# Kernel optimization log

Measured on AMD Instinct MI355X. Metric: run time of the kernel, lower is better.

The kernel has to match this reference:

```python
import jax, jax.numpy as jnp
import numpy as np
from itertools import permutations

NUM_CLASSES = 6
T_ITERS = 2
IMG = (256, 256)
EPS = 1e-12


def _pad1(x):
    # ConstantPad2d(1, 1): pad spatial dims with value 1
    return jnp.pad(x, ((0, 0), (0, 0), (1, 1), (1, 1)), constant_values=1.0)


def _maxpool3(x):
    # MaxPool2d(3, stride=1, valid) then pad(1, value=1) -> same spatial size
    y = jax.lax.reduce_window(x, -jnp.inf, jax.lax.max,
                              (1, 1, 3, 3), (1, 1, 1, 1), 'VALID')
    return _pad1(y)


def _avgpool3(x):
    y = jax.lax.reduce_window(x, 0.0, jax.lax.add,
                              (1, 1, 3, 3), (1, 1, 1, 1), 'VALID') / 9.0
    return _pad1(y)


def _normalize_ch(x):
    # F.normalize(x) default: L2 over dim=1
    n = jnp.sqrt(jnp.sum(x * x, axis=1, keepdims=True))
    return x / jnp.maximum(n, EPS)


def _opening(xp):
    # xp: [B, C2, S+2, S+2]; x = matmul(maxpool(x), xp), T times
    x = xp
    for _ in range(T_ITERS):
        x = jnp.matmul(_maxpool3(x), xp)
    return x


def _rectification(original, dilated):
    off = dilated - original
    off = off - jnp.mean(off, axis=2, keepdims=True)
    return original + jax.nn.relu(off)


def _selective_dilation(xp):
    x = xp
    for _ in range(T_ITERS):
        x2 = jnp.matmul(_avgpool3(x), xp)
        x = _rectification(x, x2)
    return x


def _final_operation(fc, mode):
    if mode == 'opening':
        operand = _pad1(-fc)            # negate-then-pad (see notes re: shape fix)
        operated = _opening(_pad1(fc))
    else:
        operand = _pad1(fc)
        operated = _selective_dilation(operand)
    x = jnp.matmul(_normalize_ch(operated), operand)
    sub = operand - x
    return jnp.sum(jnp.abs(sub))        # torch.norm(p=1)


def setup_inputs() -> dict:
    key = jax.random.key(0)
    k1, k2 = jax.random.split(key)
    logits = jax.random.normal(k1, (1, NUM_CLASSES, 64, 64), dtype=jnp.float32)
    base_loss = jax.random.uniform(k2, (1,), dtype=jnp.float32)
    return {"logits": logits, "base_loss": base_loss}


def reference(logits, base_loss):
    B, C, h, w = logits.shape
    up = jax.image.resize(logits, (B, C, IMG[0], IMG[1]), method='bilinear')
    soft = jax.nn.softmax(up, axis=1)

    # permutation pairs (i, j), i != j: cat -> mean over pair -> sub -> relu
    pairs = np.array(list(permutations(range(C), 2)))  # [P, 2]
    a = soft[:, pairs[:, 0]]            # [B, P, H, W]
    b = soft[:, pairs[:, 1]]
    d = (a - b) * 0.5                   # a - mean = (a-b)/2 ; b - mean = (b-a)/2
    fc = jnp.stack([jax.nn.relu(d), jax.nn.relu(-d)], axis=2)
    fc = fc.reshape(B, 2 * pairs.shape[0], IMG[0], IMG[1])  # [B, 2P, H, W]

    n_open = _final_operation(fc, 'opening')
    n_dil = _final_operation(fc, 'dilation')
    final_norm = jnp.abs(n_open - n_dil)
    return final_norm + base_loss       # [1]
```

## Files before the change

### kernel.cpp

```cpp
#include <hip/hip_runtime.h>
#include <math.h>

#define HP 258
#define RPAD 320
#define BSTR 328
#define NPIX (HP*HP)
#define NPB  (RPAD*BSTR)
#define PTOT (RPAD*BSTR)
#define C30 30
#define TOT (C30*NPIX)
#define LOGW 64
#define PBLK 410
#define CH 3

typedef __bf16 bf16x8 __attribute__((ext_vector_type(8)));
typedef float  f32x4  __attribute__((ext_vector_type(4)));
typedef unsigned short ushort;
typedef unsigned short ushort8 __attribute__((ext_vector_type(8)));

static __device__ inline ushort f2bf(float f){
  __bf16 h = (__bf16)f;
  return __builtin_bit_cast(ushort, h);
}
static __device__ inline float bf2f(ushort u){
  return (float)__builtin_bit_cast(__bf16, u);
}

static __device__ inline int xcd_swz(int orig, int nwg){
  int xcd = orig & 7, s = orig >> 3;
  int q = nwg >> 3, r = nwg & 7;
  return (xcd < r ? xcd*(q+1) : r*(q+1) + (xcd - r)*q) + s;
}

#define MM_MFMA_72(KK)                                                         \
  {                                                                            \
    bf16x8 a0 = __builtin_bit_cast(bf16x8, *(const ushort8*)(&As[(wr      + l15)*72 + (KK) + lq*8])); \
    bf16x8 a1 = __builtin_bit_cast(bf16x8, *(const ushort8*)(&As[(wr + 16 + l15)*72 + (KK) + lq*8])); \
    bf16x8 b0 = __builtin_bit_cast(bf16x8, *(const ushort8*)(&Bs[(wc      + l15)*72 + (KK) + lq*8])); \
    bf16x8 b1 = __builtin_bit_cast(bf16x8, *(const ushort8*)(&Bs[(wc + 16 + l15)*72 + (KK) + lq*8])); \
    acc00 = __builtin_amdgcn_mfma_f32_16x16x32_bf16(a0, b0, acc00, 0, 0, 0);   \
    acc01 = __builtin_amdgcn_mfma_f32_16x16x32_bf16(a0, b1, acc01, 0, 0, 0);   \
    acc10 = __builtin_amdgcn_mfma_f32_16x16x32_bf16(a1, b0, acc10, 0, 0, 0);   \
    acc11 = __builtin_amdgcn_mfma_f32_16x16x32_bf16(a1, b1, acc11, 0, 0, 0);   \
  }

static __device__ inline void mm_store_body(const ushort* __restrict__ Ab0,
                                            const ushort* __restrict__ Bb0,
                                            float* __restrict__ Cb,
                                            int bx, int by, int tid,
                                            ushort* As, ushort* Bs){
  int lane = tid & 63, wv = tid >> 6;
  int wr = (wv >> 1)*32, wc = (wv & 1)*32;
  int rowBase = bx*64, colBase = by*64;
  int l15 = lane & 15, lq = lane >> 4;
  f32x4 acc00 = {0.f,0.f,0.f,0.f}, acc01 = acc00, acc10 = acc00, acc11 = acc00;
  int srow = tid >> 3, sc8 = tid & 7;
  const ushort* Ab = Ab0 + (size_t)rowBase*BSTR;
  const ushort* Bb = Bb0 + (size_t)colBase*BSTR;
  const ushort* apt = Ab + (size_t)srow*BSTR + sc8*8;
  const ushort* bpt = Bb + (size_t)srow*BSTR + sc8*8;
  for (int k0 = 0; k0 < 256; k0 += 64){
    *(ushort8*)(&As[srow*72 + sc8*8])      = *(const ushort8*)(apt + k0);
    *(ushort8*)(&As[(srow+32)*72 + sc8*8]) = *(const ushort8*)(apt + (size_t)32*BSTR + k0);
    *(ushort8*)(&Bs[srow*72 + sc8*8])      = *(const ushort8*)(bpt + k0);
    *(ushort8*)(&Bs[(srow+32)*72 + sc8*8]) = *(const ushort8*)(bpt + (size_t)32*BSTR + k0);
    __syncthreads();
    MM_MFMA_72(0);
    MM_MFMA_72(32);
    __syncthreads();
  }
  {
    int row4 = tid >> 2, c84 = tid & 3;
    *(ushort8*)(&As[row4*72 + c84*8]) = *(const ushort8*)(Ab + (size_t)row4*BSTR + 256 + c84*8);
    *(ushort8*)(&Bs[row4*72 + c84*8]) = *(const ushort8*)(Bb + (size_t)row4*BSTR + 256 + c84*8);
    __syncthreads();
    MM_MFMA_72(0);
  }
  auto store = [&](f32x4 v, int r0, int c0){
    if (c0 < HP){
      #pragma unroll
      for (int r=0;r<4;r++){
        int rr = r0 + r;
        if (rr < HP) Cb[(size_t)rr*HP + c0] = v[r];
      }
    }
  };
  store(acc00, rowBase + wr +      lq*4, colBase + wc +      l15);
  store(acc01, rowBase + wr +      lq*4, colBase + wc + 16 + l15);
  store(acc10, rowBase + wr + 16 + lq*4, colBase + wc +      l15);
  store(acc11, rowBase + wr + 16 + lq*4, colBase + wc + 16 + l15);
}

static __device__ inline void mm_abs_body(bool negb,
                                          const ushort* __restrict__ Ab0,
                                          const ushort* __restrict__ Bb0,
                                          const float* __restrict__ Ob,
                                          double* __restrict__ partslot,
                                          int bx, int by, int tid,
                                          ushort* As, ushort* Bs, double* red){
  int lane = tid & 63, wv = tid >> 6;
  int wr = (wv >> 1)*32, wc = (wv & 1)*32;
  int rowBase = bx*64, colBase = by*64;
  int l15 = lane & 15, lq = lane >> 4;
  f32x4 acc00 = {0.f,0.f,0.f,0.f}, acc01 = acc00, acc10 = acc00, acc11 = acc00;
  int srow = tid >> 3, sc8 = tid & 7;
  const ushort* Ab = Ab0 + (size_t)rowBase*BSTR;
  const ushort* Bb = Bb0 + (size_t)colBase*BSTR;
  const ushort* apt = Ab + (size_t)srow*BSTR + sc8*8;
  const ushort* bpt = Bb + (size_t)srow*BSTR + sc8*8;
  ushort one = f2bf(1.0f);
  auto fixB = [&](ushort8 t8, int brow, int kbase)->ushort8{
    if (!negb) return t8;
    if (brow >= HP) return t8;
    #pragma unroll
    for (int i=0;i<8;i++){
      int kk = kbase + i;
      if (kk < HP)
        t8[i] = (brow==0 || brow==HP-1 || kk==0 || kk==HP-1) ? one : (ushort)(t8[i] ^ 0x8000);
    }
    return t8;
  };
  for (int k0 = 0; k0 < 256; k0 += 64){
    *(ushort8*)(&As[srow*72 + sc8*8])      = *(const ushort8*)(apt + k0);
    *(ushort8*)(&As[(srow+32)*72 + sc8*8]) = *(const ushort8*)(apt + (size_t)32*BSTR + k0);
    *(ushort8*)(&Bs[srow*72 + sc8*8])      = fixB(*(const ushort8*)(bpt + k0), colBase + srow, k0 + sc8*8);
    *(ushort8*)(&Bs[(srow+32)*72 + sc8*8]) = fixB(*(const ushort8*)(bpt + (size_t)32*BSTR + k0), colBase + srow + 32, k0 + sc8*8);
    __syncthreads();
    MM_MFMA_72(0);
    MM_MFMA_72(32);
    __syncthreads();
  }
  {
    int row4 = tid >> 2, c84 = tid & 3;
    *(ushort8*)(&As[row4*72 + c84*8]) = *(const ushort8*)(Ab + (size_t)row4*BSTR + 256 + c84*8);
    *(ushort8*)(&Bs[row4*72 + c84*8]) = fixB(*(const ushort8*)(Bb + (size_t)row4*BSTR + 256 + c84*8), colBase + row4, 256 + c84*8);
    __syncthreads();
    MM_MFMA_72(0);
  }
  double local = 0.0;
  auto addq = [&](f32x4 v, int r0, int c0){
    if (c0 < HP){
      #pragma unroll
      for (int r=0;r<4;r++){
        int rr = r0 + r;
        if (rr < HP){
          float o = Ob[(size_t)rr*HP + c0];
          if (negb) o = (rr==0||rr==HP-1||c0==0||c0==HP-1) ? 1.0f : -o;
          local += (double)fabsf(o - v[r]);
        }
      }
    }
  };
  addq(acc00, rowBase + wr +      lq*4, colBase + wc +      l15);
  addq(acc01, rowBase + wr +      lq*4, colBase + wc + 16 + l15);
  addq(acc10, rowBase + wr + 16 + lq*4, colBase + wc +      l15);
  addq(acc11, rowBase + wr + 16 + lq*4, colBase + wc + 16 + l15);
  red[tid] = local;
  __syncthreads();
  for (int s=128; s>0; s>>=1){ if (tid<s) red[tid]+=red[tid+s]; __syncthreads(); }
  if (tid==0) *partslot = red[0];
}

static __device__ inline void cm_body(int ch, const float* __restrict__ apart_,
                                      const float* __restrict__ xpart_,
                                      const float* __restrict__ XPd,
                                      float* __restrict__ cmo,
                                      float* colA, int tid){
  const float* ap = apart_ + (size_t)ch*10*320;
  for (int k = tid; k < HP; k += 256){
    float s = 0.0f;
    #pragma unroll
    for (int t=0;t<10;t++) s += ap[t*320 + k];
    colA[k] = s;
  }
  __syncthreads();
  const float* xpd = XPd + (size_t)ch*NPIX;
  const float* xp2 = xpart_ + (size_t)ch*10*320;
  for (int w = tid; w < HP; w += 256){
    float acc = 0.0f;
    for (int k=0;k<HP;k++) acc = fmaf(colA[k], xpd[(size_t)k*HP + w], acc);
    float xs = 0.0f;
    #pragma unroll
    for (int t=0;t<10;t++) xs += xp2[t*320 + w];
    cmo[ch*HP + w] = (acc - xs) * (1.0f/(float)HP);
  }
}

__global__ __launch_bounds__(256) void fb_buildall_k(const float* __restrict__ logits,
    float* __restrict__ XP, ushort* __restrict__ BFT,
    ushort* __restrict__ BF1, ushort* __restrict__ BF2,
    float* __restrict__ xpart, float* __restrict__ apart){
  __shared__ float s6[6][34][35];
  __shared__ float fcb[34][35];
  __shared__ ushort tbuf[32][33];
  __shared__ float cr[2][8][33];
  int tile = blockIdx.x, chunk = blockIdx.y;
  int tr = tile/10, tc = tile%10;
  int r0 = tr*32, c0 = tc*32;
  int tid = threadIdx.x;
  for (int idx = tid; idx < 34*34; idx += 256){
    int lr = idx/34, lc = idx%34;
    int h = r0 - 1 + lr, w = c0 - 1 + lc;
    float sv[6];
    if (h >= 1 && h <= 256 && w >= 1 && w <= 256){
      int oh = h-1, ow = w-1;
      float fy = 0.25f*oh - 0.375f;
      float fx = 0.25f*ow - 0.375f;
      float y0f = floorf(fy), x0f = floorf(fx);
      float ty = fy - y0f, tx2 = fx - x0f;
      int y0 = max(0, (int)y0f), y1 = min(LOGW-1, (int)y0f + 1);
      int x0 = max(0, (int)x0f), x1 = min(LOGW-1, (int)x0f + 1);
      float m = -3.402823466e+38f;
      #pragma unroll
      for (int c=0;c<6;c++){
        const float* pl = logits + c*LOGW*LOGW;
        float v00 = pl[y0*LOGW + x0], v01 = pl[y0*LOGW + x1];
        float v10 = pl[y1*LOGW + x0], v11 = pl[y1*LOGW + x1];
        float a = v00 + (v01 - v00)*tx2;
        float b = v10 + (v11 - v10)*tx2;
        float v = a + (b - a)*ty;
        sv[c] = v; m = fmaxf(m, v);
      }
      float sum = 0.0f;
      #pragma unroll
      for (int c=0;c<6;c++){ sv[c] = expf(sv[c]-m); sum += sv[c]; }
      float inv = 1.0f/sum;
      #pragma unroll
      for (int c=0;c<6;c++) sv[c] *= inv;
    } else {
      #pragma unroll
      for (int c=0;c<6;c++) sv[c] = 0.0f;
    }
    #pragma unroll
    for (int c=0;c<6;c++) s6[c][lr][lc] = sv[c];
  }
  __syncthreads();
  int tx = tid & 31, rg = tid >> 5;
  for (int cc=0; cc<CH; cc++){
    int ci = chunk*CH + cc;
    int i = ci/5, r = ci%5;
    int j = r + (r>=i ? 1 : 0);
    for (int idx = tid; idx < 34*34; idx += 256){
      int lr = idx/34, lc = idx%34;
      int h = r0 - 1 + lr, w = c0 - 1 + lc;
      float v;
      if (h < 0 || h >= HP || w < 0 || w >= HP) v = 0.0f;
      else if (h==0 || h==HP-1 || w==0 || w==HP-1) v = 1.0f;
      else v = fmaxf(0.5f*(s6[i][lr][lc] - s6[j][lr][lc]), 0.0f);
      fcb[lr][lc] = v;
    }
    __syncthreads();
    float xs_acc = 0.0f, as_acc = 0.0f;
    #pragma unroll
    for (int kk=0; kk<4; kk++){
      int lrow = rg + 8*kk;
      int h = r0 + lrow, w = c0 + tx;
      int lr = lrow + 1, lc = tx + 1;
      float xpv = fcb[lr][lc];
      ushort pmaxv, pavgv, xbfv;
      if (h >= HP || w >= HP){ pmaxv = 0; pavgv = 0; xbfv = 0; }
      else if (h==0 || h==HP-1 || w==0 || w==HP-1){
        pmaxv = f2bf(1.0f); pavgv = pmaxv; xbfv = pmaxv;
        XP[(size_t)ci*NPIX + (size_t)h*HP + w] = 1.0f;
        xs_acc += 1.0f;
        as_acc += 1.0f;
      } else {
        float mv = -3.402823466e+38f, av = 0.0f;
        #pragma unroll
        for (int dy=-1;dy<=1;dy++)
          #pragma unroll
          for (int dx=-1;dx<=1;dx++){
            float nv = fcb[lr+dy][lc+dx];
            mv = fmaxf(mv, nv); av += nv;
          }
        pmaxv = f2bf(mv);
        pavgv = f2bf(av*(1.0f/9.0f));
        xbfv  = f2bf(xpv);
        XP[(size_t)ci*NPIX + (size_t)h*HP + w] = xpv;
        xs_acc += xpv;
        as_acc += bf2f(pavgv);
      }
      size_t ob = (size_t)ci*NPB + (size_t)h*BSTR + w;
      BF1[ob] = pmaxv;
      BF2[ob] = pavgv;
      tbuf[lrow][tx] = xbfv;
    }
    cr[0][rg][tx] = xs_acc;
    cr[1][rg][tx] = as_acc;
    __syncthreads();
    if (tid < 32){
      float xs = 0.0f, as = 0.0f;
      #pragma unroll
      for (int g=0; g<8; g++){ xs += cr[0][g][tid]; as += cr[1][g][tid]; }
      xpart[((size_t)ci*10 + tr)*320 + c0 + tid] = xs;
      apart[((size_t)ci*10 + tr)*320 + c0 + tid] = as;
    }
    #pragma unroll
    for (int kk=0; kk<4; kk++){
      int a = rg + 8*kk;
      BFT[(size_t)ci*NPB + (size_t)(c0+a)*BSTR + (r0 + tx)] = tbuf[tx][a];
    }
    __syncthreads();
  }
}

__global__ __launch_bounds__(256) void fb_mm_k(const ushort* __restrict__ Aop,
    const ushort* __restrict__ Adil, const ushort* __restrict__ BT,
    float* __restrict__ Cop, float* __restrict__ Cdil,
    const float* __restrict__ XPd, const float* __restrict__ apart_,
    const float* __restrict__ xpart_, float* __restrict__ cmo){
  __shared__ ushort As[64*72];
  __shared__ ushort Bs[64*72];
  int wg = xcd_swz(blockIdx.x, 1530);
  if (wg >= 1500){
    cm_body(wg - 1500, apart_, xpart_, XPd, cmo, (float*)As, threadIdx.x);
    return;
  }
  int bx = wg % 5, by = (wg/5) % 5, z = wg/25;
  bool dil = (z >= C30);
  int ch = dil ? z - C30 : z;
  mm_store_body((dil ? Adil : Aop) + (size_t)ch*NPB, BT + (size_t)ch*NPB,
                (dil ? Cdil : Cop) + (size_t)ch*NPIX,
                bx, by, threadIdx.x, As, Bs);
}

__global__ __launch_bounds__(256) void fb_poolrect_k(const float* __restrict__ F1,
    ushort* __restrict__ BF0, const float* __restrict__ XP,
    const float* __restrict__ F2, const float* __restrict__ cm,
    float* __restrict__ X1, ushort* __restrict__ BF2,
    float* __restrict__ x1part, float* __restrict__ a2part){
  __shared__ float rect[34][35];
  __shared__ float cr2[2][8][33];
  int ci = blockIdx.y;
  int sub = blockIdx.x;
  int tid = threadIdx.x;
  if (sub < PBLK){
    int p = sub*256 + tid;
    if (p < PTOT){
      int h = p / BSTR, w = p % BSTR;
      size_t ob = (size_t)ci*NPB + p;
      if (h >= HP || w >= HP) BF0[ob] = 0;
      else if (h==0 || h==HP-1 || w==0 || w==HP-1) BF0[ob] = f2bf(1.0f);
      else {
        const float* s = F1 + (size_t)ci*NPIX;
        float mv = -3.402823466e+38f;
        #pragma unroll
        for (int dy=-1;dy<=1;dy++){
          const float* rr = s + (size_t)(h+dy)*HP + (w-1);
          mv = fmaxf(mv, fmaxf(fmaxf(rr[0],rr[1]),rr[2]));
        }
        BF0[ob] = f2bf(mv);
      }
    }
    return;
  }
  int tl = sub - PBLK;
  int tcx = tl/10, tty = tl%10;
  int c0 = tcx*32, r0 = tty*32;
  const float* xb = XP + (size_t)ci*NPIX;
  const float* yb = F2 + (size_t)ci*NPIX;
  for (int idx = tid; idx < 34*34; idx += 256){
    int lr = idx/34, lc = idx%34;
    int h = r0 - 1 + lr, w = c0 - 1 + lc;
    float v = 0.0f;
    if (h >= 0 && h < HP && w >= 0 && w < HP){
      float xv = xb[(size_t)h*HP + w];
      float off = yb[(size_t)h*HP + w] - xv - cm[ci*HP + w];
      v = xv + fmaxf(off, 0.0f);
    }
    rect[lr][lc] = v;
  }
  __syncthreads();
  int tx = tid & 31, rg = tid >> 5;
  float xs_acc = 0.0f, as_acc = 0.0f;
  #pragma unroll
  for (int kk=0; kk<4; kk++){
    int lrow = rg + 8*kk;
    int h = r0 + lrow, w = c0 + tx;
    bool vpix = (h < HP && w < HP);
    ushort o;
    if (!vpix) o = 0;
    else {
      float xv = rect[lrow+1][tx+1];
      X1[(size_t)ci*NPIX + (size_t)h*HP + w] = xv;
      xs_acc += xv;
      if (h==0 || h==HP-1 || w==0 || w==HP-1){
        o = f2bf(1.0f);
        as_acc += 1.0f;
      } else {
        float av = (rect[lrow][tx]   + rect[lrow][tx+1]   + rect[lrow][tx+2])
                 + (rect[lrow+1][tx] + rect[lrow+1][tx+1] + rect[lrow+1][tx+2])
                 + (rect[lrow+2][tx] + rect[lrow+2][tx+1] + rect[lrow+2][tx+2]);
        o = f2bf(av*(1.0f/9.0f));
        as_acc += bf2f(o);
      }
    }
    if (h < RPAD && w < 320)
      BF2[(size_t)ci*NPB + (size_t)h*BSTR + w] = o;
  }
  cr2[0][rg][tx] = xs_acc;
  cr2[1][rg][tx] = as_acc;
  __syncthreads();
  if (tid < 32){
    float xs = 0.0f, as = 0.0f;
    #pragma unroll
    for (int g=0; g<8; g++){ xs += cr2[0][g][tid]; as += cr2[1][g][tid]; }
    x1part[((size_t)ci*10 + tty)*320 + c0 + tid] = xs;
    a2part[((size_t)ci*10 + tty)*320 + c0 + tid] = as;
  }
}

__global__ __launch_bounds__(256) void fb_invrect_k(const float* __restrict__ F1,
    ushort* __restrict__ An, const float* __restrict__ X1,
    const float* __restrict__ F2, const float* __restrict__ cm,
    ushort* __restrict__ An2){
  bool second = (blockIdx.x >= PBLK);
  int p = (second ? blockIdx.x - PBLK : (int)blockIdx.x)*256 + threadIdx.x;
  if (p >= PTOT) return;
  int h = p / BSTR, w = p % BSTR;
  ushort* dst = second ? An2 : An;
  if (h >= HP || w >= HP){
    #pragma unroll
    for (int c=0;c<C30;c++) dst[(size_t)c*NPB+p] = 0;
    return;
  }
  int pd = h*HP + w;
  float v[C30];
  float ss = 0.0f;
  if (!second){
    #pragma unroll
    for (int c=0;c<C30;c++){ v[c] = F1[(size_t)c*NPIX+pd]; ss = fmaf(v[c],v[c],ss); }
  } else {
    #pragma unroll
    for (int c=0;c<C30;c++){
      float xv = X1[(size_t)c*NPIX + pd];
      float off = F2[(size_t)c*NPIX + pd] - xv - cm[c*HP + w];
      float vv = xv + fmaxf(off, 0.0f);
      v[c] = vv;
      ss = fmaf(vv, vv, ss);
    }
  }
  float n = sqrtf(2.0f*ss);
  float inv = 1.0f / fmaxf(n, 1e-12f);
  #pragma unroll
  for (int c=0;c<C30;c++) dst[(size_t)c*NPB+p] = f2bf(v[c]*inv);
}

__global__ __launch_bounds__(256) void fb_mmabs_k(const ushort* __restrict__ Aop,
    const ushort* __restrict__ Adil, const ushort* __restrict__ BT,
    const float* __restrict__ XPop, double* __restrict__ part){
  __shared__ ushort As[64*72];
  __shared__ ushort Bs[64*72];
  __shared__ double red[256];
  int wg = xcd_swz(blockIdx.x, 1500);
  int bx = wg % 5, by = (wg/5) % 5, z = wg/25;
  bool negb = (z < C30);
  int ch = negb ? z : z - C30;
  mm_abs_body(negb, (negb ? Aop : Adil) + (size_t)ch*NPB, BT + (size_t)ch*NPB,
              XPop + (size_t)ch*NPIX, &part[(size_t)z*25 + by*5 + bx],
              bx, by, threadIdx.x, As, Bs, red);
}

__global__ void fb_finalize_k(const double* __restrict__ part,
                              const float* __restrict__ base, float* __restrict__ out){
  __shared__ double s0[256], s1[256];
  int tid = threadIdx.x;
  double l0=0.0, l1=0.0;
  for (int i=tid;i<750;i+=256){ l0 += part[i]; l1 += part[750+i]; }
  s0[tid]=l0; s1[tid]=l1; __syncthreads();
  for (int s=128;s>0;s>>=1){ if (tid<s){ s0[tid]+=s0[tid+s]; s1[tid]+=s1[tid+s]; } __syncthreads(); }
  if (tid==0) out[0] = (float)(fabs(2.0*(s0[0]-s1[0])) + (double)base[0]);
}

extern "C" void kernel_launch(void* const* d_in, const int* in_sizes, int n_in,
                              void* d_out, int out_size, void* d_ws, size_t ws_size,
                              hipStream_t stream){
  const float* logits = (const float*)d_in[0];
  const float* base   = (const float*)d_in[1];
  float* out = (float*)d_out;

  char* ws = (char*)d_ws;
  size_t off = 0;
  auto alloc = [&](size_t bytes)->char*{
    char* p = ws + off; off = (off + bytes + 255) & ~(size_t)255; return p;
  };
  double* part    = (double*)alloc(1500*sizeof(double));
  float*  cm      = (float*) alloc((size_t)C30*HP*sizeof(float));
  float*  xpart   = (float*) alloc((size_t)C30*10*320*sizeof(float));
  float*  apart   = (float*) alloc((size_t)C30*10*320*sizeof(float));
  float*  x1part  = (float*) alloc((size_t)C30*10*320*sizeof(float));
  float*  a2part  = (float*) alloc((size_t)C30*10*320*sizeof(float));
  float*  XP      = (float*) alloc((size_t)TOT*sizeof(float));
  ushort* BF0     = (ushort*)alloc((size_t)C30*NPB*sizeof(ushort));
  ushort* BFT     = (ushort*)alloc((size_t)C30*NPB*sizeof(ushort));
  ushort* BF1     = (ushort*)alloc((size_t)C30*NPB*sizeof(ushort));
  ushort* BF2     = (ushort*)alloc((size_t)C30*NPB*sizeof(ushort));
  float*  F1      = (float*) alloc((size_t)TOT*sizeof(float));
  float*  F2      = (float*) alloc((size_t)TOT*sizeof(float));
  float*  X1      = (float*) alloc((size_t)TOT*sizeof(float));
  (void)ws_size; (void)in_sizes; (void)n_in; (void)out_size;

  dim3 baGrid(100, 10);
  dim3 prGrid(510, C30);

  fb_buildall_k<<<baGrid,256,0,stream>>>(logits, XP, BFT, BF1, BF2, xpart, apart);
  fb_mm_k<<<1530,256,0,stream>>>(BF1, BF2, BFT, F1, F2, XP, apart, xpart, cm);
  fb_poolrect_k<<<prGrid,256,0,stream>>>(F1, BF0, XP, F2, cm, X1, BF2, x1part, a2part);
  fb_mm_k<<<1530,256,0,stream>>>(BF0, BF2, BFT, F1, F2, XP, a2part, x1part, cm);
  fb_invrect_k<<<820,256,0,stream>>>(F1, BF1, X1, F2, cm, BF0);
  fb_mmabs_k<<<1500,256,0,stream>>>(BF1, BF0, BFT, XP, part);
  fb_finalize_k<<<1,256,0,stream>>>(part, base, out);
}
```

Baseline: 137.7 us.

## Share B tile across opening/dilation matmuls and fuse maxpool into tiled poolrect

The matmul kernel now computes the opening and dilation products for one channel in a single workgroup. It loads the shared B operand tile once and runs two sets of MFMA accumulators, which halves the grid and the B global traffic but doubles accumulator registers and LDS. The poolrect kernel drops its separate per-pixel maxpool blocks and instead computes the maxpool from an LDS-staged 34x34 tile inside the same 32x32 tile blocks. This avoids redundant global reads of neighbours at the cost of an extra sync and tile load per block.

```diff
diff --git a/kernel.cpp b/kernel.cpp
--- a/kernel.cpp
+++ b/kernel.cpp
@@ -44,39 +44,65 @@
     acc11 = __builtin_amdgcn_mfma_f32_16x16x32_bf16(a1, b1, acc11, 0, 0, 0);   \
   }
 
-static __device__ inline void mm_store_body(const ushort* __restrict__ Ab0,
-                                            const ushort* __restrict__ Bb0,
-                                            float* __restrict__ Cb,
-                                            int bx, int by, int tid,
-                                            ushort* As, ushort* Bs){
+#define MM_MFMA_PAIR(KK)                                                       \
+  {                                                                            \
+    bf16x8 b0 = __builtin_bit_cast(bf16x8, *(const ushort8*)(&Bs[(wc      + l15)*72 + (KK) + lq*8])); \
+    bf16x8 b1 = __builtin_bit_cast(bf16x8, *(const ushort8*)(&Bs[(wc + 16 + l15)*72 + (KK) + lq*8])); \
+    bf16x8 a0 = __builtin_bit_cast(bf16x8, *(const ushort8*)(&As1[(wr      + l15)*72 + (KK) + lq*8])); \
+    bf16x8 a1 = __builtin_bit_cast(bf16x8, *(const ushort8*)(&As1[(wr + 16 + l15)*72 + (KK) + lq*8])); \
+    p00 = __builtin_amdgcn_mfma_f32_16x16x32_bf16(a0, b0, p00, 0, 0, 0);       \
+    p01 = __builtin_amdgcn_mfma_f32_16x16x32_bf16(a0, b1, p01, 0, 0, 0);       \
+    p10 = __builtin_amdgcn_mfma_f32_16x16x32_bf16(a1, b0, p10, 0, 0, 0);       \
+    p11 = __builtin_amdgcn_mfma_f32_16x16x32_bf16(a1, b1, p11, 0, 0, 0);       \
+    a0 = __builtin_bit_cast(bf16x8, *(const ushort8*)(&As2[(wr      + l15)*72 + (KK) + lq*8])); \
+    a1 = __builtin_bit_cast(bf16x8, *(const ushort8*)(&As2[(wr + 16 + l15)*72 + (KK) + lq*8])); \
+    q00 = __builtin_amdgcn_mfma_f32_16x16x32_bf16(a0, b0, q00, 0, 0, 0);       \
+    q01 = __builtin_amdgcn_mfma_f32_16x16x32_bf16(a0, b1, q01, 0, 0, 0);       \
+    q10 = __builtin_amdgcn_mfma_f32_16x16x32_bf16(a1, b0, q10, 0, 0, 0);       \
+    q11 = __builtin_amdgcn_mfma_f32_16x16x32_bf16(a1, b1, q11, 0, 0, 0);       \
+  }
+
+static __device__ inline void mm_pair_body(const ushort* __restrict__ A1b,
+                                           const ushort* __restrict__ A2b,
+                                           const ushort* __restrict__ Bb0,
+                                           float* __restrict__ C1b,
+                                           float* __restrict__ C2b,
+                                           int bx, int by, int tid,
+                                           ushort* As1, ushort* As2, ushort* Bs){
   int lane = tid & 63, wv = tid >> 6;
   int wr = (wv >> 1)*32, wc = (wv & 1)*32;
   int rowBase = bx*64, colBase = by*64;
   int l15 = lane & 15, lq = lane >> 4;
-  f32x4 acc00 = {0.f,0.f,0.f,0.f}, acc01 = acc00, acc10 = acc00, acc11 = acc00;
+  f32x4 p00 = {0.f,0.f,0.f,0.f}, p01 = p00, p10 = p00, p11 = p00;
+  f32x4 q00 = p00, q01 = p00, q10 = p00, q11 = p00;
   int srow = tid >> 3, sc8 = tid & 7;
-  const ushort* Ab = Ab0 + (size_t)rowBase*BSTR;
+  const ushort* A1 = A1b + (size_t)rowBase*BSTR;
+  const ushort* A2 = A2b + (size_t)rowBase*BSTR;
   const ushort* Bb = Bb0 + (size_t)colBase*BSTR;
-  const ushort* apt = Ab + (size_t)srow*BSTR + sc8*8;
+  const ushort* a1p = A1 + (size_t)srow*BSTR + sc8*8;
+  const ushort* a2p = A2 + (size_t)srow*BSTR + sc8*8;
   const ushort* bpt = Bb + (size_t)srow*BSTR + sc8*8;
   for (int k0 = 0; k0 < 256; k0 += 64){
-    *(ushort8*)(&As[srow*72 + sc8*8])      = *(const ushort8*)(apt + k0);
-    *(ushort8*)(&As[(srow+32)*72 + sc8*8]) = *(const ushort8*)(apt + (size_t)32*BSTR + k0);
-    *(ushort8*)(&Bs[srow*72 + sc8*8])      = *(const ushort8*)(bpt + k0);
-    *(ushort8*)(&Bs[(srow+32)*72 + sc8*8]) = *(const ushort8*)(bpt + (size_t)32*BSTR + k0);
-    __syncthreads();
-    MM_MFMA_72(0);
-    MM_MFMA_72(32);
+    *(ushort8*)(&As1[srow*72 + sc8*8])      = *(const ushort8*)(a1p + k0);
+    *(ushort8*)(&As1[(srow+32)*72 + sc8*8]) = *(const ushort8*)(a1p + (size_t)32*BSTR + k0);
+    *(ushort8*)(&As2[srow*72 + sc8*8])      = *(const ushort8*)(a2p + k0);
+    *(ushort8*)(&As2[(srow+32)*72 + sc8*8]) = *(const ushort8*)(a2p + (size_t)32*BSTR + k0);
+    *(ushort8*)(&Bs[srow*72 + sc8*8])       = *(const ushort8*)(bpt + k0);
+    *(ushort8*)(&Bs[(srow+32)*72 + sc8*8])  = *(const ushort8*)(bpt + (size_t)32*BSTR + k0);
+    __syncthreads();
+    MM_MFMA_PAIR(0);
+    MM_MFMA_PAIR(32);
     __syncthreads();
   }
   {
     int row4 = tid >> 2, c84 = tid & 3;
-    *(ushort8*)(&As[row4*72 + c84*8]) = *(const ushort8*)(Ab + (size_t)row4*BSTR + 256 + c84*8);
-    *(ushort8*)(&Bs[row4*72 + c84*8]) = *(const ushort8*)(Bb + (size_t)row4*BSTR + 256 + c84*8);
-    __syncthreads();
-    MM_MFMA_72(0);
-  }
-  auto store = [&](f32x4 v, int r0, int c0){
+    *(ushort8*)(&As1[row4*72 + c84*8]) = *(const ushort8*)(A1 + (size_t)row4*BSTR + 256 + c84*8);
+    *(ushort8*)(&As2[row4*72 + c84*8]) = *(const ushort8*)(A2 + (size_t)row4*BSTR + 256 + c84*8);
+    *(ushort8*)(&Bs[row4*72 + c84*8])  = *(const ushort8*)(Bb + (size_t)row4*BSTR + 256 + c84*8);
+    __syncthreads();
+    MM_MFMA_PAIR(0);
+  }
+  auto store = [&](float* Cb, f32x4 v, int r0, int c0){
     if (c0 < HP){
       #pragma unroll
       for (int r=0;r<4;r++){
@@ -85,10 +111,14 @@
       }
     }
   };
-  store(acc00, rowBase + wr +      lq*4, colBase + wc +      l15);
-  store(acc01, rowBase + wr +      lq*4, colBase + wc + 16 + l15);
-  store(acc10, rowBase + wr + 16 + lq*4, colBase + wc +      l15);
-  store(acc11, rowBase + wr + 16 + lq*4, colBase + wc + 16 + l15);
+  store(C1b, p00, rowBase + wr +      lq*4, colBase + wc +      l15);
+  store(C1b, p01, rowBase + wr +      lq*4, colBase + wc + 16 + l15);
+  store(C1b, p10, rowBase + wr + 16 + lq*4, colBase + wc +      l15);
+  store(C1b, p11, rowBase + wr + 16 + lq*4, colBase + wc + 16 + l15);
+  store(C2b, q00, rowBase + wr +      lq*4, colBase + wc +      l15);
+  store(C2b, q01, rowBase + wr +      lq*4, colBase + wc + 16 + l15);
+  store(C2b, q10, rowBase + wr + 16 + lq*4, colBase + wc +      l15);
+  store(C2b, q11, rowBase + wr + 16 + lq*4, colBase + wc + 16 + l15);
 }
 
 static __device__ inline void mm_abs_body(bool negb,
@@ -309,19 +339,18 @@
     float* __restrict__ Cop, float* __restrict__ Cdil,
     const float* __restrict__ XPd, const float* __restrict__ apart_,
     const float* __restrict__ xpart_, float* __restrict__ cmo){
-  __shared__ ushort As[64*72];
+  __shared__ ushort As1[64*72];
+  __shared__ ushort As2[64*72];
   __shared__ ushort Bs[64*72];
-  int wg = xcd_swz(blockIdx.x, 1530);
-  if (wg >= 1500){
-    cm_body(wg - 1500, apart_, xpart_, XPd, cmo, (float*)As, threadIdx.x);
+  int wg = xcd_swz(blockIdx.x, 780);
+  if (wg >= 750){
+    cm_body(wg - 750, apart_, xpart_, XPd, cmo, (float*)As1, threadIdx.x);
     return;
   }
-  int bx = wg % 5, by = (wg/5) % 5, z = wg/25;
-  bool dil = (z >= C30);
-  int ch = dil ? z - C30 : z;
-  mm_store_body((dil ? Adil : Aop) + (size_t)ch*NPB, BT + (size_t)ch*NPB,
-                (dil ? Cdil : Cop) + (size_t)ch*NPIX,
-                bx, by, threadIdx.x, As, Bs);
+  int bx = wg % 5, by = (wg/5) % 5, ch = wg/25;
+  mm_pair_body(Aop + (size_t)ch*NPB, Adil + (size_t)ch*NPB, BT + (size_t)ch*NPB,
+               Cop + (size_t)ch*NPIX, Cdil + (size_t)ch*NPIX,
+               bx, by, threadIdx.x, As1, As2, Bs);
 }
 
 __global__ __launch_bounds__(256) void fb_poolrect_k(const float* __restrict__ F1,
@@ -332,31 +361,36 @@
   __shared__ float rect[34][35];
   __shared__ float cr2[2][8][33];
   int ci = blockIdx.y;
-  int sub = blockIdx.x;
-  int tid = threadIdx.x;
-  if (sub < PBLK){
-    int p = sub*256 + tid;
-    if (p < PTOT){
-      int h = p / BSTR, w = p % BSTR;
-      size_t ob = (size_t)ci*NPB + p;
-      if (h >= HP || w >= HP) BF0[ob] = 0;
-      else if (h==0 || h==HP-1 || w==0 || w==HP-1) BF0[ob] = f2bf(1.0f);
-      else {
-        const float* s = F1 + (size_t)ci*NPIX;
-        float mv = -3.402823466e+38f;
-        #pragma unroll
-        for (int dy=-1;dy<=1;dy++){
-          const float* rr = s + (size_t)(h+dy)*HP + (w-1);
-          mv = fmaxf(mv, fmaxf(fmaxf(rr[0],rr[1]),rr[2]));
-        }
-        BF0[ob] = f2bf(mv);
-      }
-    }
-    return;
-  }
-  int tl = sub - PBLK;
+  int tl = blockIdx.x;
   int tcx = tl/10, tty = tl%10;
   int c0 = tcx*32, r0 = tty*32;
+  int tid = threadIdx.x;
+  int tx = tid & 31, rg = tid >> 5;
+  {
+    const float* fb = F1 + (size_t)ci*NPIX;
+    for (int idx = tid; idx < 34*34; idx += 256){
+      int lr = idx/34, lc = idx%34;
+      int h = r0 - 1 + lr, w = c0 - 1 + lc;
+      rect[lr][lc] = (h >= 0 && h < HP && w >= 0 && w < HP) ? fb[(size_t)h*HP + w] : 0.0f;
+    }
+    __syncthreads();
+    #pragma unroll
+    for (int kk=0; kk<4; kk++){
+      int lrow = rg + 8*kk;
+      int h = r0 + lrow, w = c0 + tx;
+      ushort o;
+      if (h >= HP || w >= HP) o = 0;
+      else if (h==0 || h==HP-1 || w==0 || w==HP-1) o = f2bf(1.0f);
+      else {
+        float mv = fmaxf(fmaxf(rect[lrow][tx],   rect[lrow][tx+1]),   rect[lrow][tx+2]);
+        mv = fmaxf(mv, fmaxf(fmaxf(rect[lrow+1][tx], rect[lrow+1][tx+1]), rect[lrow+1][tx+2]));
+        mv = fmaxf(mv, fmaxf(fmaxf(rect[lrow+2][tx], rect[lrow+2][tx+1]), rect[lrow+2][tx+2]));
+        o = f2bf(mv);
+      }
+      BF0[(size_t)ci*NPB + (size_t)h*BSTR + w] = o;
+    }
+    __syncthreads();
+  }
   const float* xb = XP + (size_t)ci*NPIX;
   const float* yb = F2 + (size_t)ci*NPIX;
   for (int idx = tid; idx < 34*34; idx += 256){
@@ -371,7 +405,6 @@
     rect[lr][lc] = v;
   }
   __syncthreads();
-  int tx = tid & 31, rg = tid >> 5;
   float xs_acc = 0.0f, as_acc = 0.0f;
   #pragma unroll
   for (int kk=0; kk<4; kk++){
@@ -395,8 +428,7 @@
         as_acc += bf2f(o);
       }
     }
-    if (h < RPAD && w < 320)
-      BF2[(size_t)ci*NPB + (size_t)h*BSTR + w] = o;
+    BF2[(size_t)ci*NPB + (size_t)h*BSTR + w] = o;
   }
   cr2[0][rg][tx] = xs_acc;
   cr2[1][rg][tx] = as_acc;
@@ -501,12 +533,12 @@
   (void)ws_size; (void)in_sizes; (void)n_in; (void)out_size;
 
   dim3 baGrid(100, 10);
-  dim3 prGrid(510, C30);
+  dim3 prGrid(100, C30);
 
   fb_buildall_k<<<baGrid,256,0,stream>>>(logits, XP, BFT, BF1, BF2, xpart, apart);
-  fb_mm_k<<<1530,256,0,stream>>>(BF1, BF2, BFT, F1, F2, XP, apart, xpart, cm);
+  fb_mm_k<<<780,256,0,stream>>>(BF1, BF2, BFT, F1, F2, XP, apart, xpart, cm);
   fb_poolrect_k<<<prGrid,256,0,stream>>>(F1, BF0, XP, F2, cm, X1, BF2, x1part, a2part);
-  fb_mm_k<<<1530,256,0,stream>>>(BF0, BF2, BFT, F1, F2, XP, a2part, x1part, cm);
+  fb_mm_k<<<780,256,0,stream>>>(BF0, BF2, BFT, F1, F2, XP, a2part, x1part, cm);
   fb_invrect_k<<<820,256,0,stream>>>(F1, BF1, X1, F2, cm, BF0);
   fb_mmabs_k<<<1500,256,0,stream>>>(BF1, BF0, BFT, XP, part);
   fb_finalize_k<<<1,256,0,stream>>>(part, base, out);
```

Result: faster. 131.5 us (-4.5%).
